# Kernel optimization log

Hardware: AMD Instinct MI355X
Metric: run time of the kernel (lower is better)

## Reference

```python
import jax, jax.numpy as jnp
import numpy as np

NODE_ATOM = 64   # nodes per graph (fixed by layer3 Linear(1*node_atom, n_h1))
N_H1 = 1024
DIM_OUT = 128
N_NODES = 524288          # 8192 graphs * 64 nodes
N_EDGES = 16777216        # avg degree 32
BN_EPS = 1e-5


def setup_inputs() -> dict:
    key = jax.random.key(0)
    ks = jax.random.split(key, 16)
    x = jax.random.normal(ks[0], (N_NODES, 1), dtype=jnp.float32)
    edge_attr = jax.random.uniform(ks[1], (N_EDGES, 1), dtype=jnp.float32)
    edge_index = jax.random.randint(ks[2], (2, N_EDGES), 0, N_NODES, dtype=jnp.int64)
    # CGConv gated MLP params: lin_f, lin_s : Linear(2*1+1=3 -> 1)
    cg_wf = jax.random.normal(ks[3], (1, 3), dtype=jnp.float32) * 0.5
    cg_bf = jax.random.normal(ks[4], (1,), dtype=jnp.float32) * 0.1
    cg_ws = jax.random.normal(ks[5], (1, 3), dtype=jnp.float32) * 0.5
    cg_bs = jax.random.normal(ks[6], (1,), dtype=jnp.float32) * 0.1
    # GCNConv(1,1)
    gcn_w = jax.random.normal(ks[7], (1, 1), dtype=jnp.float32)
    gcn_b = jax.random.normal(ks[8], (1,), dtype=jnp.float32) * 0.1
    # MLP head
    l3_w = jax.random.normal(ks[9], (N_H1, NODE_ATOM), dtype=jnp.float32) / np.sqrt(NODE_ATOM)
    l3_b = jax.random.normal(ks[10], (N_H1,), dtype=jnp.float32) * 0.1
    bn_gamma = jnp.ones((N_H1,), dtype=jnp.float32)
    bn_beta = jnp.zeros((N_H1,), dtype=jnp.float32)
    l4_w = jax.random.normal(ks[11], (DIM_OUT, N_H1), dtype=jnp.float32) / np.sqrt(N_H1)
    l4_b = jax.random.normal(ks[12], (DIM_OUT,), dtype=jnp.float32) * 0.1
    return {"x": x, "edge_attr": edge_attr, "cg_wf": cg_wf, "cg_bf": cg_bf,
            "cg_ws": cg_ws, "cg_bs": cg_bs, "gcn_w": gcn_w, "gcn_b": gcn_b,
            "l3_w": l3_w, "l3_b": l3_b, "bn_gamma": bn_gamma, "bn_beta": bn_beta,
            "l4_w": l4_w, "l4_b": l4_b, "edge_index": edge_index}


def reference(x, edge_attr, cg_wf, cg_bf, cg_ws, cg_bs, gcn_w, gcn_b,
              l3_w, l3_b, bn_gamma, bn_beta, l4_w, l4_b, edge_index):
    n = x.shape[0]
    src = edge_index[0]  # x_j (message source)
    dst = edge_index[1]  # x_i (aggregation target)

    # ---- CGConv: z = [x_i, x_j, e]; msg = sigmoid(Wf z) * softplus(Ws z); out = x + sum_j msg
    z = jnp.concatenate([x[dst], x[src], edge_attr], axis=-1)      # [E,3]
    msg = jax.nn.sigmoid(z @ cg_wf.T + cg_bf) * jax.nn.softplus(z @ cg_ws.T + cg_bs)
    h = x + jax.ops.segment_sum(msg, dst, num_segments=n)
    h = jax.nn.relu(h)  # dropout in eval mode = identity

    # ---- GCNConv(1,1, add_self_loops=False), edge_attr used as edge_weight
    w = edge_attr[:, 0]
    deg = jax.ops.segment_sum(w, dst, num_segments=n)
    dinv = jnp.where(deg > 0, 1.0 / jnp.sqrt(jnp.maximum(deg, 1e-12)), 0.0)
    norm = dinv[src] * w * dinv[dst]                               # [E]
    hw = h @ gcn_w.T                                               # [N,1]
    h = jax.ops.segment_sum(norm[:, None] * hw[src], dst, num_segments=n) + gcn_b
    h = jax.nn.relu(h)

    # ---- to_dense_batch (uniform sorted batch) + transpose + flatten == reshape [B, node_atom]
    b = n // NODE_ATOM
    h = h.reshape(b, NODE_ATOM)

    # ---- MLP head: Linear -> BatchNorm1d (eval: running mean 0, var 1) -> relu -> Linear -> relu
    h = h @ l3_w.T + l3_b
    h = bn_gamma * h / jnp.sqrt(1.0 + BN_EPS) + bn_beta
    h = jax.nn.relu(h)
    h = jax.nn.relu(h @ l4_w.T + l4_b)
    return h
```

## Files before the change

kernel.cpp:

```cpp
#include <hip/hip_runtime.h>
#include <math.h>

#define N_NODES 524288
#define N_EDGES 16777216
#define H1      1024
#define DOUT    128

#define NB        64
#define BSH       13
#define NODES_PB  8192
#define EPB       4096
#define NBLK      (N_EDGES / EPB)
#define CAP       278528
#define PWG       8

__device__ __forceinline__ float sigmoid_f(float v) {
    return 1.0f / (1.0f + __expf(-v));
}
__device__ __forceinline__ float softplus_f(float v) {
    return fmaxf(v, 0.0f) + log1pf(__expf(-fabsf(v)));
}


__global__ __launch_bounds__(512) void a1_bin3(
    const int* __restrict__ ei, const float* __restrict__ ea,
    int* __restrict__ gcur,
    uint2* __restrict__ pkw_g)
{
    __shared__ int cnt[NB];
    __shared__ int gpos[NB];
    const int c = blockIdx.x, t = threadIdx.x;

    const int vi0 = c * 1024 + t;
    const int vi1 = vi0 + 512;
    const int4 s4a = ((const int4*)ei)[vi0];
    const int4 s4b = ((const int4*)ei)[vi1];
    const int4 d4a = ((const int4*)(ei + N_EDGES))[vi0];
    const int4 d4b = ((const int4*)(ei + N_EDGES))[vi1];
    const float4 w4a = ((const float4*)ea)[vi0];
    const float4 w4b = ((const float4*)ea)[vi1];
    int srcs[8], dsts[8];
    float ws[8];
    srcs[0]=s4a.x; srcs[1]=s4a.y; srcs[2]=s4a.z; srcs[3]=s4a.w;
    srcs[4]=s4b.x; srcs[5]=s4b.y; srcs[6]=s4b.z; srcs[7]=s4b.w;
    dsts[0]=d4a.x; dsts[1]=d4a.y; dsts[2]=d4a.z; dsts[3]=d4a.w;
    dsts[4]=d4b.x; dsts[5]=d4b.y; dsts[6]=d4b.z; dsts[7]=d4b.w;
    ws[0]=w4a.x; ws[1]=w4a.y; ws[2]=w4a.z; ws[3]=w4a.w;
    ws[4]=w4b.x; ws[5]=w4b.y; ws[6]=w4b.z; ws[7]=w4b.w;

    if (t < NB) cnt[t] = 0;
    __syncthreads();

    int rank[8];
#pragma unroll
    for (int q = 0; q < 8; ++q)
        rank[q] = atomicAdd(&cnt[dsts[q] >> BSH], 1);
    __syncthreads();

    if (t < NB) gpos[t] = atomicAdd(&gcur[t * 16], cnt[t]);
    __syncthreads();

#pragma unroll
    for (int q = 0; q < 8; ++q) {
        const int dst = dsts[q];
        const int b = dst >> BSH;
        const size_t slot = (size_t)b * CAP + gpos[b] + rank[q];
        const unsigned int pk = ((unsigned int)srcs[q] << 13) |
                                (unsigned int)(dst & (NODES_PB - 1));
        pkw_g[slot] = make_uint2(pk, __float_as_uint(ws[q]));
    }
}

__global__ __launch_bounds__(1024) void b1_accum(
    const uint2* __restrict__ pkw_g, const int* __restrict__ gcur,
    const float* __restrict__ x,
    const float* __restrict__ cg_wf, const float* __restrict__ cg_bf,
    const float* __restrict__ cg_ws, const float* __restrict__ cg_bs,
    float* __restrict__ part1)
{
    __shared__ float lm[NODES_PB];
    __shared__ float ld[NODES_PB];
    const int b = blockIdx.x / PWG, p = blockIdx.x % PWG;
    for (int i = threadIdx.x; i < NODES_PB; i += 1024) { lm[i] = 0.0f; ld[i] = 0.0f; }
    __syncthreads();
    const float wf0 = cg_wf[0], wf1 = cg_wf[1], wf2 = cg_wf[2], bf = cg_bf[0];
    const float s0c = cg_ws[0], s1c = cg_ws[1], s2c = cg_ws[2], bsc = cg_bs[0];
    const float* xb = x + (size_t)b * NODES_PB;
    const int tot = gcur[b * 16];
    const int per = (tot + PWG - 1) / PWG;
    const int s0 = p * per;
    const int s1 = min(tot, s0 + per);
    const size_t gb = (size_t)b * CAP;
    for (int k = s0 + (int)threadIdx.x; k < s1; k += 1024) {
        const uint2 v = pkw_g[gb + k];
        const int dl = v.x & (NODES_PB - 1);
        const int src = v.x >> 13;
        const float w = __uint_as_float(v.y);
        const float xs = x[src];
        const float xd = xb[dl];
        const float f = fmaf(wf0, xd, fmaf(wf1, xs, fmaf(wf2, w, bf)));
        const float sv = fmaf(s0c, xd, fmaf(s1c, xs, fmaf(s2c, w, bsc)));
        const float msg = sigmoid_f(f) * softplus_f(sv);
        atomicAdd(&lm[dl], msg);
        atomicAdd(&ld[dl], w);
    }
    __syncthreads();
    float* pm = part1 + (size_t)(b * PWG + p) * NODES_PB;
    float* pd = part1 + (size_t)NB * PWG * NODES_PB + (size_t)(b * PWG + p) * NODES_PB;
    for (int k = threadIdx.x; k < NODES_PB; k += 1024) { pm[k] = lm[k]; pd[k] = ld[k]; }
}

__global__ __launch_bounds__(256) void c1_nodemid(
    const float* __restrict__ part1, const float* __restrict__ x,
    const float* __restrict__ gcn_w,
    float* __restrict__ dinv, float* __restrict__ a)
{
    const int n = blockIdx.x * 256 + threadIdx.x;
    const int b = n >> BSH, dl = n & (NODES_PB - 1);
    const float* pm = part1 + (size_t)b * PWG * NODES_PB + dl;
    const float* pd = part1 + (size_t)NB * PWG * NODES_PB + (size_t)b * PWG * NODES_PB + dl;
    float m = 0.0f, d = 0.0f;
#pragma unroll
    for (int p = 0; p < PWG; ++p) {
        m += pm[(size_t)p * NODES_PB];
        d += pd[(size_t)p * NODES_PB];
    }
    const float h = fmaxf(x[n] + m, 0.0f);
    const float di = (d > 0.0f) ? (1.0f / sqrtf(fmaxf(d, 1e-12f))) : 0.0f;
    dinv[n] = di;
    a[n] = di * h * gcn_w[0];
}

__global__ __launch_bounds__(1024) void b2_accum(
    const uint2* __restrict__ pkw_g, const int* __restrict__ gcur,
    const float* __restrict__ a, float* __restrict__ part2)
{
    __shared__ float ls[NODES_PB];
    const int b = blockIdx.x / PWG, p = blockIdx.x % PWG;
    for (int i = threadIdx.x; i < NODES_PB; i += 1024) ls[i] = 0.0f;
    __syncthreads();
    const int tot = gcur[b * 16];
    const int per = (tot + PWG - 1) / PWG;
    const int s0 = p * per;
    const int s1 = min(tot, s0 + per);
    const size_t gb = (size_t)b * CAP;
    for (int k = s0 + (int)threadIdx.x; k < s1; k += 1024) {
        const uint2 v = pkw_g[gb + k];
        atomicAdd(&ls[v.x & (NODES_PB - 1)], a[v.x >> 13] * __uint_as_float(v.y));
    }
    __syncthreads();
    float* ps = part2 + (size_t)(b * PWG + p) * NODES_PB;
    for (int k = threadIdx.x; k < NODES_PB; k += 1024) ps[k] = ls[k];
}

__global__ __launch_bounds__(256) void c2_nodefin(
    const float* __restrict__ part2, const float* __restrict__ dinv,
    const float* __restrict__ gcn_b, float* __restrict__ hfin)
{
    const int n = blockIdx.x * 256 + threadIdx.x;
    const int b = n >> BSH, dl = n & (NODES_PB - 1);
    const float* ps = part2 + (size_t)b * PWG * NODES_PB + dl;
    float s = 0.0f;
#pragma unroll
    for (int p = 0; p < PWG; ++p) s += ps[(size_t)p * NODES_PB];
    hfin[n] = fmaxf(fmaf(dinv[n], s, gcn_b[0]), 0.0f);
}


__global__ __launch_bounds__(256) void edge_pass1(
    const int* __restrict__ ei, const float* __restrict__ ea,
    const float* __restrict__ x,
    const float* __restrict__ cg_wf, const float* __restrict__ cg_bf,
    const float* __restrict__ cg_ws, const float* __restrict__ cg_bs,
    float* __restrict__ msg_sum, float* __restrict__ deg)
{
    const float wf0 = cg_wf[0], wf1 = cg_wf[1], wf2 = cg_wf[2], bf = cg_bf[0];
    const float s0 = cg_ws[0], s1 = cg_ws[1], s2 = cg_ws[2], bs = cg_bs[0];
    const int t = blockIdx.x * 256 + threadIdx.x;
    const int4 src4 = ((const int4*)ei)[t];
    const int4 dst4 = ((const int4*)(ei + N_EDGES))[t];
    const float4 w4 = ((const float4*)ea)[t];
    const int* sp = (const int*)&src4;
    const int* dp = (const int*)&dst4;
    const float* wp = (const float*)&w4;
#pragma unroll
    for (int q = 0; q < 4; ++q) {
        const int src = sp[q], dst = dp[q];
        const float w = wp[q];
        const float xs = x[src], xd = x[dst];
        const float f = fmaf(wf0, xd, fmaf(wf1, xs, fmaf(wf2, w, bf)));
        const float s = fmaf(s0, xd, fmaf(s1, xs, fmaf(s2, w, bs)));
        const float msg = sigmoid_f(f) * softplus_f(s);
        unsafeAtomicAdd(&msg_sum[dst], msg);
        unsafeAtomicAdd(&deg[dst], w);
    }
}

__global__ __launch_bounds__(256) void node_mid(
    const float* __restrict__ x, const float* __restrict__ msg_sum,
    float* __restrict__ deg_dinv, float* __restrict__ a,
    const float* __restrict__ gcn_w)
{
    const int i = blockIdx.x * 256 + threadIdx.x;
    const float gw = gcn_w[0];
    const float h = fmaxf(x[i] + msg_sum[i], 0.0f);
    const float d = deg_dinv[i];
    const float dinv = (d > 0.0f) ? (1.0f / sqrtf(fmaxf(d, 1e-12f))) : 0.0f;
    deg_dinv[i] = dinv;
    a[i] = dinv * h * gw;
}

__global__ __launch_bounds__(256) void edge_pass2(
    const int* __restrict__ ei, const float* __restrict__ ea,
    const float* __restrict__ a, float* __restrict__ s)
{
    const int t = blockIdx.x * 256 + threadIdx.x;
    const int4 src4 = ((const int4*)ei)[t];
    const int4 dst4 = ((const int4*)(ei + N_EDGES))[t];
    const float4 w4 = ((const float4*)ea)[t];
    const int* sp = (const int*)&src4;
    const int* dp = (const int*)&dst4;
    const float* wp = (const float*)&w4;
#pragma unroll
    for (int q = 0; q < 4; ++q)
        unsafeAtomicAdd(&s[dp[q]], a[sp[q]] * wp[q]);
}

__global__ __launch_bounds__(256) void node_fin(
    const float* __restrict__ dinv, const float* __restrict__ s,
    const float* __restrict__ gcn_b, float* __restrict__ hfin)
{
    const int i = blockIdx.x * 256 + threadIdx.x;
    hfin[i] = fmaxf(fmaf(dinv[i], s[i], gcn_b[0]), 0.0f);
}


__global__ __launch_bounds__(256) void fold_bn(
    const float* __restrict__ l3_w, const float* __restrict__ l3_b,
    const float* __restrict__ g, const float* __restrict__ be,
    float* __restrict__ w3f, float* __restrict__ b3f)
{
    const int idx = blockIdx.x * 256 + threadIdx.x;
    const int j = idx >> 6, k = idx & 63;
    const float invs = 1.0f / sqrtf(1.0f + 1e-5f);
    const float sc = g[j] * invs;
    w3f[idx] = l3_w[idx] * sc;
    if (k == 0) b3f[j] = fmaf(l3_b[j], sc, be[j]);
}

__global__ __launch_bounds__(256) void gemm1(
    const float* __restrict__ A, const float* __restrict__ W,
    const float* __restrict__ bias, float* __restrict__ C)
{
    __shared__ float As[64][68];
    __shared__ float Ws[64][68];
    const int bj = blockIdx.x, bi = blockIdx.y;
    const int t = threadIdx.x;
#pragma unroll
    for (int q2 = 0; q2 < 4; ++q2) {
        const int idx = t + 256 * q2;
        const int r = idx >> 4, c = idx & 15;
        const float4 va = *(const float4*)(A + (size_t)(bi * 64 + r) * 64 + c * 4);
        const float4 vw = *(const float4*)(W + (size_t)(bj * 64 + r) * 64 + c * 4);
        As[c*4+0][r] = va.x; As[c*4+1][r] = va.y; As[c*4+2][r] = va.z; As[c*4+3][r] = va.w;
        Ws[c*4+0][r] = vw.x; Ws[c*4+1][r] = vw.y; Ws[c*4+2][r] = vw.z; Ws[c*4+3][r] = vw.w;
    }
    __syncthreads();
    const int tx = t & 15, ty = t >> 4;
    const int i0 = ty * 4, j0 = tx * 4;
    float acc[4][4] = {};
#pragma unroll 16
    for (int k = 0; k < 64; ++k) {
        const float4 av = *(const float4*)&As[k][i0];
        const float4 wv = *(const float4*)&Ws[k][j0];
        const float* ap = (const float*)&av;
        const float* wp = (const float*)&wv;
#pragma unroll
        for (int ii = 0; ii < 4; ++ii)
#pragma unroll
            for (int jj = 0; jj < 4; ++jj)
                acc[ii][jj] = fmaf(ap[ii], wp[jj], acc[ii][jj]);
    }
    const int gj = bj * 64 + j0;
    const float4 bv = *(const float4*)(bias + gj);
#pragma unroll
    for (int ii = 0; ii < 4; ++ii) {
        const int gi = bi * 64 + i0 + ii;
        float4 o;
        o.x = fmaxf(acc[ii][0] + bv.x, 0.0f);
        o.y = fmaxf(acc[ii][1] + bv.y, 0.0f);
        o.z = fmaxf(acc[ii][2] + bv.z, 0.0f);
        o.w = fmaxf(acc[ii][3] + bv.w, 0.0f);
        *(float4*)(C + (size_t)gi * H1 + gj) = o;
    }
}

__global__ __launch_bounds__(256) void gemm2(
    const float* __restrict__ H, const float* __restrict__ W,
    const float* __restrict__ bias, float* __restrict__ O)
{
    __shared__ float Hs[64][36];
    __shared__ float Ws[64][132];
    const int bi = blockIdx.x;
    const int t = threadIdx.x;
    const int tx = t & 31, ty = t >> 5;
    const int i0 = ty * 4, j0 = tx * 4;
    float acc[4][4] = {};
    for (int kc = 0; kc < H1; kc += 64) {
#pragma unroll
        for (int q2 = 0; q2 < 2; ++q2) {
            const int idx = t + 256 * q2;
            const int r = idx >> 4, c = idx & 15;
            const float4 v = *(const float4*)(H + (size_t)(bi * 32 + r) * H1 + kc + c * 4);
            Hs[c*4+0][r] = v.x; Hs[c*4+1][r] = v.y; Hs[c*4+2][r] = v.z; Hs[c*4+3][r] = v.w;
        }
#pragma unroll
        for (int q2 = 0; q2 < 8; ++q2) {
            const int idx = t + 256 * q2;
            const int r = idx >> 4, c = idx & 15;
            const float4 v = *(const float4*)(W + (size_t)r * H1 + kc + c * 4);
            Ws[c*4+0][r] = v.x; Ws[c*4+1][r] = v.y; Ws[c*4+2][r] = v.z; Ws[c*4+3][r] = v.w;
        }
        __syncthreads();
#pragma unroll 16
        for (int k = 0; k < 64; ++k) {
            const float4 hv = *(const float4*)&Hs[k][i0];
            const float4 wv = *(const float4*)&Ws[k][j0];
            const float* hp = (const float*)&hv;
            const float* wp = (const float*)&wv;
#pragma unroll
            for (int ii = 0; ii < 4; ++ii)
#pragma unroll
                for (int jj = 0; jj < 4; ++jj)
                    acc[ii][jj] = fmaf(hp[ii], wp[jj], acc[ii][jj]);
        }
        __syncthreads();
    }
    const float4 bv = *(const float4*)(bias + j0);
#pragma unroll
    for (int ii = 0; ii < 4; ++ii) {
        const int gi = bi * 32 + i0 + ii;
        float4 o;
        o.x = fmaxf(acc[ii][0] + bv.x, 0.0f);
        o.y = fmaxf(acc[ii][1] + bv.y, 0.0f);
        o.z = fmaxf(acc[ii][2] + bv.z, 0.0f);
        o.w = fmaxf(acc[ii][3] + bv.w, 0.0f);
        *(float4*)(O + (size_t)gi * DOUT + j0) = o;
    }
}


extern "C" void kernel_launch(void* const* d_in, const int* in_sizes, int n_in,
                              void* d_out, int out_size, void* d_ws, size_t ws_size,
                              hipStream_t stream) {
    const float* x     = (const float*)d_in[0];
    const float* ea    = (const float*)d_in[1];
    const float* cg_wf = (const float*)d_in[2];
    const float* cg_bf = (const float*)d_in[3];
    const float* cg_ws = (const float*)d_in[4];
    const float* cg_bs = (const float*)d_in[5];
    const float* gcn_w = (const float*)d_in[6];
    const float* gcn_b = (const float*)d_in[7];
    const float* l3_w  = (const float*)d_in[8];
    const float* l3_b  = (const float*)d_in[9];
    const float* bn_g  = (const float*)d_in[10];
    const float* bn_b  = (const float*)d_in[11];
    const float* l4_w  = (const float*)d_in[12];
    const float* l4_b  = (const float*)d_in[13];
    const int*   ei    = (const int*)d_in[14];
    float* out = (float*)d_out;
    char* ws = (char*)d_ws;

    const size_t off_pkw   = 0;
    const size_t off_gcur  = off_pkw + (size_t)NB * CAP * 8;
    const size_t off_p1    = off_gcur + 4096;
    const size_t off_p2    = off_p1 + (size_t)NB * PWG * NODES_PB * 2 * 4;
    const size_t off_dinv  = off_p2 + (size_t)NB * PWG * NODES_PB * 4;
    const size_t off_a     = off_dinv + (size_t)N_NODES * 4;
    const size_t off_hfin  = off_a + (size_t)N_NODES * 4;
    const size_t off_h3    = off_hfin + (size_t)N_NODES * 4;
    const size_t off_w3    = off_h3 + (size_t)8192 * H1 * 4;
    const size_t off_b3    = off_w3 + (size_t)H1 * 64 * 4;
    const size_t required  = off_b3 + (size_t)H1 * 4;

    if (ws_size >= required) {
        uint2* pkw   = (uint2*)(ws + off_pkw);
        int*   gcur  = (int*)(ws + off_gcur);
        float* p1    = (float*)(ws + off_p1);
        float* p2    = (float*)(ws + off_p2);
        float* dinv  = (float*)(ws + off_dinv);
        float* a     = (float*)(ws + off_a);
        float* hfin  = (float*)(ws + off_hfin);
        float* h3    = (float*)(ws + off_h3);
        float* w3    = (float*)(ws + off_w3);
        float* b3    = (float*)(ws + off_b3);

        hipMemsetAsync(gcur, 0, 4096, stream);
        fold_bn<<<256, 256, 0, stream>>>(l3_w, l3_b, bn_g, bn_b, w3, b3);
        a1_bin3<<<NBLK, 512, 0, stream>>>(ei, ea, gcur, pkw);
        b1_accum<<<NB * PWG, 1024, 0, stream>>>(pkw, gcur, x,
                                                cg_wf, cg_bf, cg_ws, cg_bs, p1);
        c1_nodemid<<<N_NODES / 256, 256, 0, stream>>>(p1, x, gcn_w, dinv, a);
        b2_accum<<<NB * PWG, 1024, 0, stream>>>(pkw, gcur, a, p2);
        c2_nodefin<<<N_NODES / 256, 256, 0, stream>>>(p2, dinv, gcn_b, hfin);
        gemm1<<<dim3(16, 128), 256, 0, stream>>>(hfin, w3, b3, h3);
        gemm2<<<256, 256, 0, stream>>>(h3, l4_w, l4_b, out);
    } else {
        float* buf_msg  = (float*)(ws + 0);
        float* buf_deg  = (float*)(ws + (size_t)2097152);
        float* buf_a    = (float*)(ws + (size_t)4194304);
        float* buf_hfin = (float*)(ws + (size_t)6291456);
        float* buf_h3   = (float*)(ws + (size_t)8388608);
        float* buf_w3   = (float*)(ws + (size_t)41943040);
        float* buf_b3   = (float*)(ws + (size_t)42205184);

        hipMemsetAsync(buf_msg, 0, (size_t)N_NODES * 4, stream);
        hipMemsetAsync(buf_deg, 0, (size_t)N_NODES * 4, stream);
        fold_bn<<<256, 256, 0, stream>>>(l3_w, l3_b, bn_g, bn_b, buf_w3, buf_b3);
        edge_pass1<<<N_EDGES / 4 / 256, 256, 0, stream>>>(
            ei, ea, x, cg_wf, cg_bf, cg_ws, cg_bs, buf_msg, buf_deg);
        node_mid<<<N_NODES / 256, 256, 0, stream>>>(x, buf_msg, buf_deg, buf_a, gcn_w);
        hipMemsetAsync(buf_msg, 0, (size_t)N_NODES * 4, stream);
        edge_pass2<<<N_EDGES / 4 / 256, 256, 0, stream>>>(ei, ea, buf_a, buf_msg);
        node_fin<<<N_NODES / 256, 256, 0, stream>>>(buf_deg, buf_msg, gcn_b, buf_hfin);
        gemm1<<<dim3(16, 128), 256, 0, stream>>>(buf_hfin, buf_w3, buf_b3, buf_h3);
        gemm2<<<256, 256, 0, stream>>>(buf_h3, l4_w, l4_b, out);
    }
}
```

Baseline: 688.2 us.

## Use finer destination bins and paired 16-byte edge loads in accumulation kernels

Doubles the number of destination bins so each bin covers 4096 nodes. This halves the LDS per accumulation block and allows more resident blocks. The binning kernel now handles 8192 edges per 1024-thread block. Both accumulation kernels read two packed edges per 16-byte load using evenly aligned partitions, which reduces load instruction count at the cost of more partial buffers and atomics on a smaller LDS table.

```diff
diff --git a/kernel.cpp b/kernel.cpp
--- a/kernel.cpp
+++ b/kernel.cpp
@@ -6,12 +6,12 @@
 #define H1      1024
 #define DOUT    128
 
-#define NB        64
-#define BSH       13
-#define NODES_PB  8192
-#define EPB       4096
+#define NB        128
+#define BSH       12
+#define NODES_PB  4096
+#define EPB       8192
 #define NBLK      (N_EDGES / EPB)
-#define CAP       278528
+#define CAP       139264
 #define PWG       8
 
 __device__ __forceinline__ float sigmoid_f(float v) {
@@ -22,7 +22,7 @@
 }
 
 
-__global__ __launch_bounds__(512) void a1_bin3(
+__global__ __launch_bounds__(1024) void a1_bin4(
     const int* __restrict__ ei, const float* __restrict__ ea,
     int* __restrict__ gcur,
     uint2* __restrict__ pkw_g)
@@ -31,8 +31,8 @@
     __shared__ int gpos[NB];
     const int c = blockIdx.x, t = threadIdx.x;
 
-    const int vi0 = c * 1024 + t;
-    const int vi1 = vi0 + 512;
+    const int vi0 = c * 2048 + t;
+    const int vi1 = vi0 + 1024;
     const int4 s4a = ((const int4*)ei)[vi0];
     const int4 s4b = ((const int4*)ei)[vi1];
     const int4 d4a = ((const int4*)(ei + N_EDGES))[vi0];
@@ -65,13 +65,13 @@
         const int dst = dsts[q];
         const int b = dst >> BSH;
         const size_t slot = (size_t)b * CAP + gpos[b] + rank[q];
-        const unsigned int pk = ((unsigned int)srcs[q] << 13) |
+        const unsigned int pk = ((unsigned int)srcs[q] << 12) |
                                 (unsigned int)(dst & (NODES_PB - 1));
         pkw_g[slot] = make_uint2(pk, __float_as_uint(ws[q]));
     }
 }
 
-__global__ __launch_bounds__(1024) void b1_accum(
+__global__ __launch_bounds__(512) void b1_accum(
     const uint2* __restrict__ pkw_g, const int* __restrict__ gcur,
     const float* __restrict__ x,
     const float* __restrict__ cg_wf, const float* __restrict__ cg_bf,
@@ -81,33 +81,54 @@
     __shared__ float lm[NODES_PB];
     __shared__ float ld[NODES_PB];
     const int b = blockIdx.x / PWG, p = blockIdx.x % PWG;
-    for (int i = threadIdx.x; i < NODES_PB; i += 1024) { lm[i] = 0.0f; ld[i] = 0.0f; }
+    for (int i = threadIdx.x; i < NODES_PB; i += 512) { lm[i] = 0.0f; ld[i] = 0.0f; }
     __syncthreads();
     const float wf0 = cg_wf[0], wf1 = cg_wf[1], wf2 = cg_wf[2], bf = cg_bf[0];
     const float s0c = cg_ws[0], s1c = cg_ws[1], s2c = cg_ws[2], bsc = cg_bs[0];
     const float* xb = x + (size_t)b * NODES_PB;
     const int tot = gcur[b * 16];
-    const int per = (tot + PWG - 1) / PWG;
+    const int per = (((tot + PWG - 1) / PWG) + 1) & ~1;
     const int s0 = p * per;
     const int s1 = min(tot, s0 + per);
-    const size_t gb = (size_t)b * CAP;
-    for (int k = s0 + (int)threadIdx.x; k < s1; k += 1024) {
-        const uint2 v = pkw_g[gb + k];
-        const int dl = v.x & (NODES_PB - 1);
-        const int src = v.x >> 13;
-        const float w = __uint_as_float(v.y);
-        const float xs = x[src];
-        const float xd = xb[dl];
-        const float f = fmaf(wf0, xd, fmaf(wf1, xs, fmaf(wf2, w, bf)));
-        const float sv = fmaf(s0c, xd, fmaf(s1c, xs, fmaf(s2c, w, bsc)));
-        const float msg = sigmoid_f(f) * softplus_f(sv);
-        atomicAdd(&lm[dl], msg);
-        atomicAdd(&ld[dl], w);
+    const uint2* base = pkw_g + (size_t)b * CAP;
+    if (s1 > s0) {
+        const int npair = (s1 - s0) >> 1;
+        const uint4* v4 = (const uint4*)(base + s0);
+#pragma unroll 2
+        for (int k = threadIdx.x; k < npair; k += 512) {
+            const uint4 r = v4[k];
+            const int dl0 = r.x & (NODES_PB - 1), src0 = r.x >> BSH;
+            const int dl1 = r.z & (NODES_PB - 1), src1 = r.z >> BSH;
+            const float w0 = __uint_as_float(r.y), w1 = __uint_as_float(r.w);
+            const float xs0 = x[src0], xs1 = x[src1];
+            const float xd0 = xb[dl0], xd1 = xb[dl1];
+            const float f0 = fmaf(wf0, xd0, fmaf(wf1, xs0, fmaf(wf2, w0, bf)));
+            const float g0 = fmaf(s0c, xd0, fmaf(s1c, xs0, fmaf(s2c, w0, bsc)));
+            const float f1 = fmaf(wf0, xd1, fmaf(wf1, xs1, fmaf(wf2, w1, bf)));
+            const float g1 = fmaf(s0c, xd1, fmaf(s1c, xs1, fmaf(s2c, w1, bsc)));
+            const float m0 = sigmoid_f(f0) * softplus_f(g0);
+            const float m1 = sigmoid_f(f1) * softplus_f(g1);
+            atomicAdd(&lm[dl0], m0);
+            atomicAdd(&ld[dl0], w0);
+            atomicAdd(&lm[dl1], m1);
+            atomicAdd(&ld[dl1], w1);
+        }
+        for (int k = s0 + (npair << 1) + (int)threadIdx.x; k < s1; k += 512) {
+            const uint2 v = base[k];
+            const int dl = v.x & (NODES_PB - 1);
+            const int src = v.x >> BSH;
+            const float w = __uint_as_float(v.y);
+            const float xs = x[src], xd = xb[dl];
+            const float f = fmaf(wf0, xd, fmaf(wf1, xs, fmaf(wf2, w, bf)));
+            const float g = fmaf(s0c, xd, fmaf(s1c, xs, fmaf(s2c, w, bsc)));
+            atomicAdd(&lm[dl], sigmoid_f(f) * softplus_f(g));
+            atomicAdd(&ld[dl], w);
+        }
     }
     __syncthreads();
     float* pm = part1 + (size_t)(b * PWG + p) * NODES_PB;
     float* pd = part1 + (size_t)NB * PWG * NODES_PB + (size_t)(b * PWG + p) * NODES_PB;
-    for (int k = threadIdx.x; k < NODES_PB; k += 1024) { pm[k] = lm[k]; pd[k] = ld[k]; }
+    for (int k = threadIdx.x; k < NODES_PB; k += 512) { pm[k] = lm[k]; pd[k] = ld[k]; }
 }
 
 __global__ __launch_bounds__(256) void c1_nodemid(
@@ -131,26 +152,38 @@
     a[n] = di * h * gcn_w[0];
 }
 
-__global__ __launch_bounds__(1024) void b2_accum(
+__global__ __launch_bounds__(512) void b2_accum(
     const uint2* __restrict__ pkw_g, const int* __restrict__ gcur,
     const float* __restrict__ a, float* __restrict__ part2)
 {
     __shared__ float ls[NODES_PB];
     const int b = blockIdx.x / PWG, p = blockIdx.x % PWG;
-    for (int i = threadIdx.x; i < NODES_PB; i += 1024) ls[i] = 0.0f;
+    for (int i = threadIdx.x; i < NODES_PB; i += 512) ls[i] = 0.0f;
     __syncthreads();
     const int tot = gcur[b * 16];
-    const int per = (tot + PWG - 1) / PWG;
+    const int per = (((tot + PWG - 1) / PWG) + 1) & ~1;
     const int s0 = p * per;
     const int s1 = min(tot, s0 + per);
-    const size_t gb = (size_t)b * CAP;
-    for (int k = s0 + (int)threadIdx.x; k < s1; k += 1024) {
-        const uint2 v = pkw_g[gb + k];
-        atomicAdd(&ls[v.x & (NODES_PB - 1)], a[v.x >> 13] * __uint_as_float(v.y));
+    const uint2* base = pkw_g + (size_t)b * CAP;
+    if (s1 > s0) {
+        const int npair = (s1 - s0) >> 1;
+        const uint4* v4 = (const uint4*)(base + s0);
+#pragma unroll 2
+        for (int k = threadIdx.x; k < npair; k += 512) {
+            const uint4 r = v4[k];
+            const float a0 = a[r.x >> BSH];
+            const float a1 = a[r.z >> BSH];
+            atomicAdd(&ls[r.x & (NODES_PB - 1)], a0 * __uint_as_float(r.y));
+            atomicAdd(&ls[r.z & (NODES_PB - 1)], a1 * __uint_as_float(r.w));
+        }
+        for (int k = s0 + (npair << 1) + (int)threadIdx.x; k < s1; k += 512) {
+            const uint2 v = base[k];
+            atomicAdd(&ls[v.x & (NODES_PB - 1)], a[v.x >> BSH] * __uint_as_float(v.y));
+        }
     }
     __syncthreads();
     float* ps = part2 + (size_t)(b * PWG + p) * NODES_PB;
-    for (int k = threadIdx.x; k < NODES_PB; k += 1024) ps[k] = ls[k];
+    for (int k = threadIdx.x; k < NODES_PB; k += 512) ps[k] = ls[k];
 }
 
 __global__ __launch_bounds__(256) void c2_nodefin(
@@ -373,7 +406,7 @@
 
     const size_t off_pkw   = 0;
     const size_t off_gcur  = off_pkw + (size_t)NB * CAP * 8;
-    const size_t off_p1    = off_gcur + 4096;
+    const size_t off_p1    = off_gcur + 8192;
     const size_t off_p2    = off_p1 + (size_t)NB * PWG * NODES_PB * 2 * 4;
     const size_t off_dinv  = off_p2 + (size_t)NB * PWG * NODES_PB * 4;
     const size_t off_a     = off_dinv + (size_t)N_NODES * 4;
@@ -395,13 +428,13 @@
         float* w3    = (float*)(ws + off_w3);
         float* b3    = (float*)(ws + off_b3);
 
-        hipMemsetAsync(gcur, 0, 4096, stream);
+        hipMemsetAsync(gcur, 0, 8192, stream);
         fold_bn<<<256, 256, 0, stream>>>(l3_w, l3_b, bn_g, bn_b, w3, b3);
-        a1_bin3<<<NBLK, 512, 0, stream>>>(ei, ea, gcur, pkw);
-        b1_accum<<<NB * PWG, 1024, 0, stream>>>(pkw, gcur, x,
-                                                cg_wf, cg_bf, cg_ws, cg_bs, p1);
+        a1_bin4<<<NBLK, 1024, 0, stream>>>(ei, ea, gcur, pkw);
+        b1_accum<<<NB * PWG, 512, 0, stream>>>(pkw, gcur, x,
+                                               cg_wf, cg_bf, cg_ws, cg_bs, p1);
         c1_nodemid<<<N_NODES / 256, 256, 0, stream>>>(p1, x, gcn_w, dinv, a);
-        b2_accum<<<NB * PWG, 1024, 0, stream>>>(pkw, gcur, a, p2);
+        b2_accum<<<NB * PWG, 512, 0, stream>>>(pkw, gcur, a, p2);
         c2_nodefin<<<N_NODES / 256, 256, 0, stream>>>(p2, dinv, gcn_b, hfin);
         gemm1<<<dim3(16, 128), 256, 0, stream>>>(hfin, w3, b3, h3);
         gemm2<<<256, 256, 0, stream>>>(h3, l4_w, l4_b, out);
```

Result: no change. 682.5 us (-0.8%).
